# Optimization experiments

Measured on AMD Instinct MI355X. Metric: run time of the kernel, lower is better.

Reference implementation:

```python
import jax, jax.numpy as jnp
import numpy as np

HEADS, KDIM, VDIM = 8, 32, 64  # ImageLinearAttention defaults
EPS = 1e-8

def lrelu(x):
    return jax.nn.leaky_relu(x, 0.2)

def up2(x):
    # torch nn.Upsample(scale_factor=2, mode='bilinear', align_corners=False)
    b, c, h, w = x.shape
    return jax.image.resize(x, (b, c, 2 * h, 2 * w), method='bilinear')

def blur(x):
    # normalized [1,2,1] outer-product depthwise blur (kornia filter2d, normalized=True)
    c = x.shape[1]
    f = jnp.array([1.0, 2.0, 1.0], dtype=x.dtype)
    k = (f[:, None] * f[None, :]) / 16.0
    kern = jnp.broadcast_to(k, (c, 1, 3, 3))
    return jax.lax.conv_general_dilated(x, kern, (1, 1), [(1, 1), (1, 1)], feature_group_count=c)

def conv2dmod(x, W, y, demod):
    # x [b,ci,h,w], W [co,ci,k,k], y [b,ci]; per-sample modulated (de)conv
    w = W[None] * (y[:, None, :, None, None] + 1.0)  # [b,co,ci,k,k]
    if demod:
        d = jax.lax.rsqrt(jnp.sum(w * w, axis=(2, 3, 4), keepdims=True) + EPS)
        w = w * d
    pad = (W.shape[-1] - 1) // 2  # same padding, stride=1, dilation=1
    conv1 = lambda xi, wi: jax.lax.conv_general_dilated(xi[None], wi, (1, 1), [(pad, pad), (pad, pad)])[0]
    return jax.vmap(conv1)(x, w)

def attn_and_ff(x, qw, kw, vw, ow, ob, ga, f1w, f1b, f2w, f2b, gf):
    # Residual(Rezero(ImageLinearAttention)) then Residual(Rezero(conv1x1-leaky-conv1x1))
    b, c, h, w = x.shape
    n = h * w
    xf = x.reshape(b, c, n)
    scale = KDIM ** -0.25
    q = (jnp.einsum('dc,bcn->bdn', qw, xf) * scale).reshape(b, HEADS, KDIM, n)
    k = (jnp.einsum('dc,bcn->bdn', kw, xf) * scale).reshape(b, HEADS, KDIM, n)
    v = jnp.einsum('dc,bcn->bdn', vw, xf).reshape(b, HEADS, VDIM, n)
    k = jax.nn.softmax(k, axis=-1)          # over pixels
    q = jax.nn.softmax(q, axis=-2)          # norm_queries: over key dim
    ctx = jnp.einsum('bhdn,bhen->bhde', k, v)
    out = jnp.einsum('bhdn,bhde->bhen', q, ctx).reshape(b, HEADS * VDIM, n)
    out = jnp.einsum('cd,bdn->bcn', ow, out) + ob[None, :, None]
    x = x + ga * out.reshape(b, c, h, w)
    h1 = lrelu(jnp.einsum('dc,bcn->bdn', f1w, x.reshape(b, c, n)) + f1b[None, :, None])
    ff = jnp.einsum('cd,bdn->bcn', f2w, h1) + f2b[None, :, None]
    return x + gf * ff.reshape(b, c, h, w)

def setup_inputs() -> dict:
    key = jax.random.key(0)
    ks = jax.random.split(key, 20)
    B, CIN, F, L, H, W = 4, 128, 64, 512, 64, 64
    DK, DV = HEADS * KDIM, HEADS * VDIM
    d = {}
    d['x'] = jax.random.normal(ks[0], (B, CIN, H, W), jnp.float32)
    d['prev_rgb'] = jax.random.normal(ks[1], (B, 3, 2 * H, 2 * W), jnp.float32)
    d['istyle'] = jax.random.normal(ks[2], (B, L), jnp.float32)
    d['noise1'] = jax.random.normal(ks[3], (B, F, 2 * H, 2 * W), jnp.float32)
    d['noise2'] = jax.random.normal(ks[4], (B, F, 2 * H, 2 * W), jnp.float32)
    d['conv1_w'] = jax.random.normal(ks[5], (F, CIN, 3, 3), jnp.float32) * (2.0 / (CIN * 9)) ** 0.5
    d['conv2_w'] = jax.random.normal(ks[6], (F, F, 3, 3), jnp.float32) * (2.0 / (F * 9)) ** 0.5
    d['style_w'] = jax.random.normal(ks[7], (F, L), jnp.float32) * L ** -0.5
    d['style_b'] = jnp.zeros((F,), jnp.float32)
    d['rgb_w'] = jax.random.normal(ks[8], (3, F, 1, 1), jnp.float32) * (2.0 / F) ** 0.5
    d['qw'] = jax.random.normal(ks[9], (2, DK, F), jnp.float32) * F ** -0.5
    d['kw'] = jax.random.normal(ks[10], (2, DK, F), jnp.float32) * F ** -0.5
    d['vw'] = jax.random.normal(ks[11], (2, DV, F), jnp.float32) * F ** -0.5
    d['ow'] = jax.random.normal(ks[12], (2, F, DV), jnp.float32) * DV ** -0.5
    d['ob'] = jnp.zeros((2, F), jnp.float32)
    d['ga'] = 0.1 * jnp.ones((2,), jnp.float32)  # rezero gate (nonzero for a meaningful baseline)
    d['f1w'] = jax.random.normal(ks[13], (2, 2 * F, F), jnp.float32) * F ** -0.5
    d['f1b'] = jnp.zeros((2, 2 * F), jnp.float32)
    d['f2w'] = jax.random.normal(ks[14], (2, F, 2 * F), jnp.float32) * (2 * F) ** -0.5
    d['f2b'] = jnp.zeros((2, F), jnp.float32)
    d['gf'] = 0.1 * jnp.ones((2,), jnp.float32)
    return d

def reference(x, prev_rgb, istyle, noise1, noise2, conv1_w, conv2_w, style_w, style_b, rgb_w,
              qw, kw, vw, ow, ob, ga, f1w, f1b, f2w, f2b, gf):
    b = x.shape[0]
    x = up2(x)
    n1 = attn_and_ff(noise1, qw[0], kw[0], vw[0], ow[0], ob[0], ga[0], f1w[0], f1b[0], f2w[0], f2b[0], gf[0])
    n2 = attn_and_ff(noise2, qw[1], kw[1], vw[1], ow[1], ob[1], ga[1], f1w[1], f1b[1], f2w[1], f2b[1], gf[1])
    ones1 = jnp.ones((b, conv1_w.shape[1]), x.dtype)  # style1 = ones
    x = lrelu(conv2dmod(x, conv1_w, ones1, True) + n1)
    ones2 = jnp.ones((b, conv2_w.shape[1]), x.dtype)  # style2 = ones
    x = lrelu(conv2dmod(x, conv2_w, ones2, True) + n2)
    style = istyle @ style_w.T + style_b             # RGBBlock.to_style
    rgb = conv2dmod(x, rgb_w, style, False) + prev_rgb
    rgb = blur(up2(rgb))                             # upsample_rgb: bilinear x2 + blur
    return (x, rgb)
```

## Files before the change

kernel.cpp:

```cpp
#include <hip/hip_runtime.h>
#include <math.h>

#define NB 4
#define NF 64
#define NPIX 16384
#define DK 256
#define DV 512
#define QKSCALE 0.4204482f

typedef __attribute__((ext_vector_type(8))) short bf16x8;
typedef __attribute__((ext_vector_type(4))) float f32x4;
#define MFMA16(a, b, c) __builtin_amdgcn_mfma_f32_16x16x32_bf16(a, b, c, 0, 0, 0)

__device__ __forceinline__ short f2bf(float f) {
  __bf16 h = (__bf16)f;
  return __builtin_bit_cast(short, h);
}
__device__ __forceinline__ float bf2f(short s) {
  unsigned u = ((unsigned)(unsigned short)s) << 16;
  return __builtin_bit_cast(float, u);
}

#define OFF_XUPT   0L
#define OFF_XAT    4194304L
#define OFF_NBT    6291456L
#define OFF_NZT    10485760L
#define OFF_GPART  14680064L
#define OFF_WB1    25165824L
#define OFF_WB2    25202688L
#define OFF_STYLE  25221120L
#define OFF_RGBS   25221376L
#define OFF_QWB    25417984L
#define OFF_KWB    25434368L
#define OFF_F1WB   25450752L
#define OFF_F2WB   25458944L
#define OFF_MTT    25467136L
#define OFF_GSUM   25532672L

#define CDIV(a,b) (((a)+(b)-1)/(b))

__global__ void cvt4_kernel(const float* __restrict__ qw, const float* __restrict__ kw,
                            const float* __restrict__ f1w, const float* __restrict__ f2w,
                            short* __restrict__ qwP, short* __restrict__ kwP,
                            short* __restrict__ f1P, short* __restrict__ f2P,
                            const float* __restrict__ istyle, const float* __restrict__ sw,
                            const float* __restrict__ sb, float* __restrict__ styleb) {
  if (blockIdx.x == 384) {
    int b = threadIdx.x >> 6;
    int c = threadIdx.x & 63;
    float a = 0.f;
    const float* ip = istyle + b * 512;
    const float* wp = sw + c * 512;
    for (int l = 0; l < 512; ++l) a += ip[l] * wp[l];
    styleb[b * 64 + c] = a + sb[c];
    return;
  }
  int i = blockIdx.x * 256 + threadIdx.x;
  if (i < 32768) {
    int i_t = i >> 14, rem = i & 16383;
    int hd = rem >> 10, ks = (rem >> 9) & 1, lane = (rem >> 3) & 63, j = rem & 7;
    int l15 = lane & 15, quad = lane >> 4;
    qwP[i] = f2bf(qw[i_t * 16384 + (hd * 16 + l15) * 64 + ks * 32 + quad * 8 + j]);
  } else if (i < 65536) {
    int ii = i - 32768;
    int i_t = ii >> 14, rem = ii & 16383;
    int q = rem >> 12, dt = (rem >> 10) & 3, ks = (rem >> 9) & 1, lane = (rem >> 3) & 63, j = rem & 7;
    int l15 = lane & 15, quad = lane >> 4;
    kwP[ii] = f2bf(kw[i_t * 16384 + (q * 64 + dt * 16 + l15) * 64 + ks * 32 + quad * 8 + j]);
  } else if (i < 81920) {
    int ii = i - 65536;
    int i_t = ii >> 13, rem = ii & 8191;
    int jt = rem >> 10, ks = (rem >> 9) & 1, lane = (rem >> 3) & 63, j = rem & 7;
    int l15 = lane & 15, quad = lane >> 4;
    f1P[ii] = f2bf(f1w[i_t * 8192 + (jt * 16 + l15) * 64 + ks * 32 + quad * 8 + j]);
  } else {
    int ii = i - 81920;
    int i_t = ii >> 13, rem = ii & 8191;
    int ct = rem >> 11, p = (rem >> 10) & 1, ks = (rem >> 9) & 1, lane = (rem >> 3) & 63, j = rem & 7;
    int l15 = lane & 15, quad = lane >> 4;
    f2P[ii] = f2bf(f2w[i_t * 8192 + (ct * 16 + l15) * 128 + p * 64 + ks * 32 + quad * 8 + j]);
  }
}

__global__ __launch_bounds__(256) void up2t_kernel(const float* __restrict__ in,
                                                   short* __restrict__ outT) {
  __shared__ float row[64 * 132];
  int b = blockIdx.y, y = blockIdx.x, tid = threadIdx.x;
  int w = tid >> 6, lane = tid & 63, quad = lane >> 4, l15 = lane & 15;
  float iy = y * 0.5f - 0.25f;
  int y0 = (int)floorf(iy); float wy = iy - (float)y0;
  int ylo = y0 < 0 ? 0 : y0;
  int yhi = y0 + 1 > 63 ? 63 : y0 + 1;
  for (int it = 0; it < 32; ++it) {
    int idx = it * 256 + tid;
    int c = idx >> 6, xin = idx & 63;
    const float* bp = in + ((long)(b * 128 + c)) * 4096;
    float v0 = bp[ylo * 64 + xin];
    float v1 = bp[yhi * 64 + xin];
    row[xin * 132 + c] = (1.f - wy) * v0 + wy * v1;
  }
  __syncthreads();
  long ybase = (((long)(b * 128 + y)) * 128) * 128;
#pragma unroll
  for (int s = 0; s < 8; ++s) {
    int x = w * 32 + s * 4 + quad;
    float ix = x * 0.5f - 0.25f;
    int x0 = (int)floorf(ix); float wx = ix - (float)x0;
    int xlo = x0 < 0 ? 0 : x0;
    int xhi = x0 + 1 > 63 ? 63 : x0 + 1;
    bf16x8 pack;
#pragma unroll
    for (int j = 0; j < 8; ++j) {
      int c = l15 * 8 + j;
      float v = (1.f - wx) * row[xlo * 132 + c] + wx * row[xhi * 132 + c];
      pack[j] = f2bf(v);
    }
    *(bf16x8*)(outT + ybase + (long)x * 128 + l15 * 8) = pack;
  }
}

__global__ __launch_bounds__(256) void nzt_kernel(const float* __restrict__ nz1,
                                                  const float* __restrict__ nz2,
                                                  short* __restrict__ nzP) {
  __shared__ short tile[64 * 264];
  int i = blockIdx.z, b = blockIdx.y;
  long n0 = (long)blockIdx.x * 256;
  const float* nz = (i == 0) ? nz1 : nz2;
  int tid = threadIdx.x;
  const float* src = nz + (long)b * 64 * NPIX + n0;
#pragma unroll
  for (int k = 0; k < 16; ++k) {
    int idx = tid + k * 256;
    int c = idx >> 6, g = idx & 63;
    float4 v = *(const float4*)(src + (long)c * NPIX + g * 4);
    short* tp = tile + c * 264 + g * 4;
    tp[0] = f2bf(v.x); tp[1] = f2bf(v.y); tp[2] = f2bf(v.z); tp[3] = f2bf(v.w);
  }
  __syncthreads();
  long fragb = ((long)(i * NB + b)) * 1024 + blockIdx.x * 16;
#pragma unroll
  for (int v = 0; v < 8; ++v) {
    int slot = tid + v * 256;
    int frag = slot >> 6, lane = slot & 63;
    int nt = frag >> 1, ks = frag & 1;
    int l15 = lane & 15, quad = lane >> 4;
    bf16x8 pack;
#pragma unroll
    for (int j = 0; j < 8; ++j)
      pack[j] = tile[(ks * 32 + quad * 8 + j) * 264 + nt * 16 + l15];
    *(bf16x8*)(nzP + ((fragb + nt) * 2 + ks) * 512 + lane * 8) = pack;
  }
}

__global__ void wnorm2_kernel(const float* __restrict__ W1, const float* __restrict__ W2,
                              short* __restrict__ wb1, short* __restrict__ wb2) {
  int which = blockIdx.x >> 6;
  int co = blockIdx.x & 63;
  const float* W = which ? W2 : W1;
  short* wbP = which ? wb2 : wb1;
  int CI = which ? 64 : 128;
  int n = CI * 9;
  int KS = CI >> 5;
  __shared__ float red[256];
  float s = 0.f;
  for (int idx = threadIdx.x; idx < n; idx += 256) {
    float w2 = 2.0f * W[co * n + idx];
    s += w2 * w2;
  }
  red[threadIdx.x] = s;
  __syncthreads();
  for (int off = 128; off > 0; off >>= 1) {
    if (threadIdx.x < off) red[threadIdx.x] += red[threadIdx.x + off];
    __syncthreads();
  }
  float sc = rsqrtf(red[0] + 1e-8f);
  int ct = co >> 4, l15 = co & 15;
  for (int idx = threadIdx.x; idx < n; idx += 256) {
    int ci = idx / 9, k = idx - ci * 9;
    int ks = ci >> 5, quad = (ci >> 3) & 3, j = ci & 7;
    wbP[((k * 4 + ct) * KS + ks) * 512 + (quad * 16 + l15) * 8 + j] =
        f2bf(2.0f * W[co * n + idx] * sc);
  }
}

__global__ __launch_bounds__(256, 4) void pk_kernel(const float* __restrict__ nz1,
                                                    const float* __restrict__ nz2,
                                                    const short* __restrict__ nzP,
                                                    const short* __restrict__ kwP,
                                                    short* __restrict__ Gpartb) {
  __shared__ __attribute__((aligned(16))) char lds[39168];
  int bi = blockIdx.x, ch = blockIdx.y;
  int i = bi >> 2, b = bi & 3;
  const float* nz = (i == 0) ? nz1 : nz2;
  const short* kwP_i = kwP + i * (DK * NF);
  int tid = threadIdx.x;
  int w = tid >> 6, lane = tid & 63, quad = lane >> 4, l15 = lane & 15;
  int n0 = ch * 128;
  short* Xb = (short*)lds;
  short* Ph = (short*)(lds + 21760);
#pragma unroll
  for (int k = 0; k < 8; ++k) {
    int idx = tid + k * 256;
    int c = idx >> 5, g = idx & 31;
    float4 v = *(const float4*)(nz + ((long)b * 64 + c) * NPIX + n0 + g * 4);
    short* xp = Xb + c * 136 + g * 4;
    xp[0] = f2bf(v.x); xp[1] = f2bf(v.y); xp[2] = f2bf(v.z); xp[3] = f2bf(v.w);
  }
  for (int k = 0; k < 8; ++k) {
    int idx = tid + k * 256;
    int c = 64 + (idx >> 7), n = idx & 127;
    Xb[c * 136 + n] = (c == 64) ? (short)0x3F80 : (short)0;
  }
  bf16x8 bfr[2][2];
#pragma unroll
  for (int j = 0; j < 2; ++j)
#pragma unroll
    for (int ks = 0; ks < 2; ++ks)
      bfr[j][ks] = *(const bf16x8*)(nzP +
          (((long)bi * 1024 + ch * 8 + 2 * w + j) * 2 + ks) * 512 + lane * 8);
  __syncthreads();
  for (int q = 0; q < 4; ++q) {
    f32x4 acc[2][4];
#pragma unroll
    for (int j = 0; j < 2; ++j)
#pragma unroll
      for (int dt = 0; dt < 4; ++dt) acc[j][dt] = (f32x4){0.f, 0.f, 0.f, 0.f};
#pragma unroll
    for (int j = 0; j < 2; ++j) {
#pragma unroll
      for (int ks = 0; ks < 2; ++ks) {
#pragma unroll
        for (int dt = 0; dt < 4; ++dt) {
          bf16x8 afr = *(const bf16x8*)(kwP_i + (((q * 4 + dt) * 2 + ks) * 512 + lane * 8));
          acc[j][dt] = MFMA16(afr, bfr[j][ks], acc[j][dt]);
        }
      }
    }
#pragma unroll
    for (int j = 0; j < 2; ++j) {
      int ntile = 2 * w + j;
#pragma unroll
      for (int dt = 0; dt < 4; ++dt)
#pragma unroll
        for (int r = 0; r < 4; ++r) {
          float p = __expf(acc[j][dt][r] * QKSCALE);
          Ph[(dt * 16 + quad * 4 + r) * 136 + ntile * 16 + l15] = f2bf(p);
        }
    }
    __syncthreads();
#pragma unroll
    for (int ct = 0; ct < 5; ++ct) {
      f32x4 g = (f32x4){0.f, 0.f, 0.f, 0.f};
#pragma unroll
      for (int ks = 0; ks < 4; ++ks) {
        bf16x8 afr = *(const bf16x8*)(Ph + (w * 16 + l15) * 136 + ks * 32 + quad * 8);
        bf16x8 bfr2 = *(const bf16x8*)(Xb + (ct * 16 + l15) * 136 + ks * 32 + quad * 8);
        g = MFMA16(afr, bfr2, g);
      }
#pragma unroll
      for (int r = 0; r < 4; ++r) {
        int row = q * 64 + w * 16 + quad * 4 + r;
        Gpartb[(((long)bi * 128 + ch) * 256 + row) * 80 + ct * 16 + l15] = f2bf(g[r]);
      }
    }
    __syncthreads();
  }
}

__global__ __launch_bounds__(256) void gsum_kernel(const short* __restrict__ Gpartb,
                                                   float* __restrict__ Gsum) {
  int idx4 = blockIdx.x * 256 + threadIdx.x;
  int bi = idx4 / 5120;
  int rem4 = idx4 - bi * 5120;
  const short* gp = Gpartb + (long)bi * 128 * 20480 + rem4 * 4;
  float a0 = 0.f, a1 = 0.f, a2 = 0.f, a3 = 0.f;
#pragma unroll 8
  for (int ch = 0; ch < 128; ++ch) {
    short4 v = *(const short4*)(gp + (long)ch * 20480);
    a0 += bf2f(v.x); a1 += bf2f(v.y); a2 += bf2f(v.z); a3 += bf2f(v.w);
  }
  float4 o = {a0, a1, a2, a3};
  *(float4*)(Gsum + (long)bi * 20480 + rem4 * 4) = o;
}

__global__ __launch_bounds__(256) void ctxM_kernel(const float* __restrict__ Gsum,
                                                   const float* __restrict__ vw,
                                                   const float* __restrict__ ow,
                                                   short* __restrict__ MtP) {
  int i = blockIdx.z, b = blockIdx.y, dt = blockIdx.x * 16;
  int h = dt >> 5;
  __shared__ float Gs[16][81];
  __shared__ float ctxs[16][68];
  int t = threadIdx.x;
  const float* gsb = Gsum + ((long)(i * NB + b)) * 20480;
  for (int idx = t; idx < 1280; idx += 256) {
    int dl = idx / 80, c = idx - dl * 80;
    Gs[dl][c] = gsb[(dt + dl) * 80 + c];
  }
  __syncthreads();
  const float* vw_i = vw + (long)i * DV * NF;
  const float* ow_i = ow + (long)i * NF * DV;
  for (int idx = t; idx < 1024; idx += 256) {
    int dl = idx & 15, e = idx >> 4;
    const float* vp = vw_i + (h * 64 + e) * 64;
    float a = 0.f;
#pragma unroll
    for (int c = 0; c < 64; ++c) a += Gs[dl][c] * vp[c];
    ctxs[dl][e] = a / Gs[dl][64];
  }
  __syncthreads();
  short* mtp = MtP + ((long)(i * NB + b)) * 16384;
  for (int idx = t; idx < 1024; idx += 256) {
    int dl = idx & 15, c = idx >> 4;
    const float* op = ow_i + c * 512 + h * 64;
    float a = 0.f;
#pragma unroll
    for (int e = 0; e < 64; ++e) a += op[e] * ctxs[dl][e];
    int d = dt + dl;
    int ct = c >> 4, l15 = c & 15, hh = d >> 5, quad = (d >> 3) & 3, r = d & 7;
    mtp[((ct * 8 + hh) * 64 + quad * 16 + l15) * 8 + r] = f2bf(a);
  }
}

__global__ __launch_bounds__(256, 6) void attnd4_kernel(
    const short* __restrict__ nzP, const short* __restrict__ qwP,
    const short* __restrict__ MtP, const float* __restrict__ ob,
    const float* __restrict__ gap, const short* __restrict__ f1P,
    const float* __restrict__ f1b, const short* __restrict__ f2P,
    const float* __restrict__ f2b, const float* __restrict__ gfp,
    short* __restrict__ noutP) {
  __shared__ __attribute__((aligned(16))) short lds[4 * 2048];
  int bi = blockIdx.x;
  int i = bi >> 2;
  int tid = threadIdx.x;
  int w = tid >> 6, lane = tid & 63, quad = lane >> 4, l15 = lane & 15;
  short* Xt = lds + w * 2048;
  short* Es = Xt + 1152;
  float ga = gap[i], gf = gfp[i];
  const short* qwP_i = qwP + i * (DK * NF);
  const short* f1P_i = f1P + i * (128 * 64);
  const float* f1b_i = f1b + i * 128;
  const short* f2P_i = f2P + i * (64 * 128);
  const float* f2b_i = f2b + i * 64;
  const float* ob_i = ob + i * 64;
  long ntile = (long)bi * 1024 + blockIdx.y * 4 + w;
  const short* nb = nzP + ntile * 1024;
  bf16x8 xfr0 = *(const bf16x8*)(nb + lane * 8);
  bf16x8 xfr1 = *(const bf16x8*)(nb + 512 + lane * 8);
  *(bf16x8*)(Xt + l15 * 72 + quad * 8) = xfr0;
  *(bf16x8*)(Xt + l15 * 72 + 32 + quad * 8) = xfr1;
  const short* mtp = MtP + (long)bi * 16384;
  f32x4 acc2[4];
#pragma unroll
  for (int ct = 0; ct < 4; ++ct) acc2[ct] = (f32x4){0.f, 0.f, 0.f, 0.f};
#pragma unroll
  for (int h = 0; h < 8; ++h) {
    f32x4 q[2];
#pragma unroll
    for (int dd = 0; dd < 2; ++dd) {
      int hd = 2 * h + dd;
      q[dd] = (f32x4){0.f, 0.f, 0.f, 0.f};
      bf16x8 a0 = *(const bf16x8*)(qwP_i + (hd * 2 + 0) * 512 + lane * 8);
      q[dd] = MFMA16(a0, xfr0, q[dd]);
      bf16x8 a1 = *(const bf16x8*)(qwP_i + (hd * 2 + 1) * 512 + lane * 8);
      q[dd] = MFMA16(a1, xfr1, q[dd]);
    }
    float part = 0.f;
#pragma unroll
    for (int dd = 0; dd < 2; ++dd)
#pragma unroll
      for (int r = 0; r < 4; ++r) {
        float e = __expf(q[dd][r] * QKSCALE);
        q[dd][r] = e;
        part += e;
      }
    float p2 = part + __shfl_xor(part, 16);
    float s = p2 + __shfl_xor(p2, 32);
    float inv = 1.0f / s;
#pragma unroll
    for (int dd = 0; dd < 2; ++dd) {
      short4 ev;
      ev.x = f2bf(q[dd][0] * inv); ev.y = f2bf(q[dd][1] * inv);
      ev.z = f2bf(q[dd][2] * inv); ev.w = f2bf(q[dd][3] * inv);
      *(short4*)(Es + l15 * 56 + dd * 16 + quad * 4) = ev;
    }
    bf16x8 efr = *(const bf16x8*)(Es + l15 * 56 + quad * 8);
#pragma unroll
    for (int ct = 0; ct < 4; ++ct) {
      bf16x8 afr = *(const bf16x8*)(mtp + (ct * 8 + h) * 512 + lane * 8);
      acc2[ct] = MFMA16(afr, efr, acc2[ct]);
    }
  }
  float yreg[4][4];
#pragma unroll
  for (int ct = 0; ct < 4; ++ct) {
    int c0 = ct * 16 + quad * 4;
    short4 xs = *(const short4*)(Xt + l15 * 72 + c0);
    float xv[4] = {bf2f(xs.x), bf2f(xs.y), bf2f(xs.z), bf2f(xs.w)};
    short4 ys;
#pragma unroll
    for (int r = 0; r < 4; ++r) yreg[ct][r] = xv[r] + ga * (acc2[ct][r] + ob_i[c0 + r]);
    ys.x = f2bf(yreg[ct][0]); ys.y = f2bf(yreg[ct][1]);
    ys.z = f2bf(yreg[ct][2]); ys.w = f2bf(yreg[ct][3]);
    *(short4*)(Xt + l15 * 72 + c0) = ys;
  }
  bf16x8 yfr0 = *(const bf16x8*)(Xt + l15 * 72 + quad * 8);
  bf16x8 yfr1 = *(const bf16x8*)(Xt + l15 * 72 + 32 + quad * 8);
  f32x4 acc3[8];
#pragma unroll
  for (int jt = 0; jt < 8; ++jt) {
    acc3[jt] = (f32x4){0.f, 0.f, 0.f, 0.f};
    bf16x8 a0 = *(const bf16x8*)(f1P_i + (jt * 2 + 0) * 512 + lane * 8);
    acc3[jt] = MFMA16(a0, yfr0, acc3[jt]);
    bf16x8 a1 = *(const bf16x8*)(f1P_i + (jt * 2 + 1) * 512 + lane * 8);
    acc3[jt] = MFMA16(a1, yfr1, acc3[jt]);
  }
  f32x4 acc4[4];
#pragma unroll
  for (int ct = 0; ct < 4; ++ct) acc4[ct] = (f32x4){0.f, 0.f, 0.f, 0.f};
#pragma unroll
  for (int p = 0; p < 2; ++p) {
#pragma unroll
    for (int jj = 0; jj < 4; ++jj) {
      int jt = p * 4 + jj;
      short4 hs;
#pragma unroll
      for (int r = 0; r < 4; ++r) {
        float a = acc3[jt][r] + f1b_i[jt * 16 + quad * 4 + r];
        a = a > 0.f ? a : 0.2f * a;
        ((short*)&hs)[r] = f2bf(a);
      }
      *(short4*)(Xt + l15 * 72 + jj * 16 + quad * 4) = hs;
    }
    bf16x8 h0 = *(const bf16x8*)(Xt + l15 * 72 + quad * 8);
    bf16x8 h1 = *(const bf16x8*)(Xt + l15 * 72 + 32 + quad * 8);
#pragma unroll
    for (int ct = 0; ct < 4; ++ct) {
      bf16x8 a0 = *(const bf16x8*)(f2P_i + ((ct * 2 + p) * 2 + 0) * 512 + lane * 8);
      acc4[ct] = MFMA16(a0, h0, acc4[ct]);
      bf16x8 a1 = *(const bf16x8*)(f2P_i + ((ct * 2 + p) * 2 + 1) * 512 + lane * 8);
      acc4[ct] = MFMA16(a1, h1, acc4[ct]);
    }
  }
#pragma unroll
  for (int ct = 0; ct < 4; ++ct) {
    int c0 = ct * 16 + quad * 4;
    short4 ov;
#pragma unroll
    for (int r = 0; r < 4; ++r)
      ((short*)&ov)[r] = f2bf(yreg[ct][r] + gf * (acc4[ct][r] + f2b_i[c0 + r]));
    *(short4*)(noutP + (ntile * 4 + ct) * 256 + lane * 4) = ov;
  }
}

__global__ __launch_bounds__(256, 4) void convmfma_kernel(
    const short* __restrict__ inT, int CI, const short* __restrict__ wbP,
    const short* __restrict__ addnP, float* __restrict__ out_nchw,
    short* __restrict__ out_nhwc, const float* __restrict__ rgbw,
    const float* __restrict__ styleb, const float* __restrict__ prev,
    float* __restrict__ rgbs) {
  __shared__ __attribute__((aligned(16))) short Bs[3 * 66 * 40];
  int xh = blockIdx.x, y = blockIdx.y, b = blockIdx.z;
  int tid = threadIdx.x;
  int w = tid >> 6, lane = tid & 63, quad = lane >> 4, l15 = lane & 15;
  int KS = CI >> 5;
  f32x4 acc[4];
#pragma unroll
  for (int ct = 0; ct < 4; ++ct) acc[ct] = (f32x4){0.f, 0.f, 0.f, 0.f};
  for (int ks = 0; ks < KS; ++ks) {
    if (ks) __syncthreads();
    for (int t = tid; t < 792; t += 256) {
      int ci8 = t & 3, xr = t >> 2;
      int xi = xr % 66, r = xr / 66;
      int gy = y + r - 1, gx = xh * 64 + xi - 1;
      bf16x8 v = {0, 0, 0, 0, 0, 0, 0, 0};
      if (gy >= 0 && gy < 128 && gx >= 0 && gx < 128)
        v = *(const bf16x8*)(inT + (((long)(b * 128 + gy)) * 128 + gx) * CI + ks * 32 + ci8 * 8);
      *(bf16x8*)(Bs + (r * 66 + xi) * 40 + ci8 * 8) = v;
    }
    __syncthreads();
#pragma unroll
    for (int sh = 0; sh < 9; ++sh) {
      int dyv = sh / 3, dxv = sh - dyv * 3;
      const short* wbase = wbP + ((sh * 4) * KS + ks) * 512 + lane * 8;
      bf16x8 a0 = *(const bf16x8*)(wbase);
      bf16x8 a1 = *(const bf16x8*)(wbase + KS * 512);
      bf16x8 a2 = *(const bf16x8*)(wbase + 2 * KS * 512);
      bf16x8 a3 = *(const bf16x8*)(wbase + 3 * KS * 512);
      int xi = w * 16 + l15 + dxv;
      bf16x8 bf = *(const bf16x8*)(Bs + (dyv * 66 + xi) * 40 + quad * 8);
      acc[0] = MFMA16(a0, bf, acc[0]);
      acc[1] = MFMA16(a1, bf, acc[1]);
      acc[2] = MFMA16(a2, bf, acc[2]);
      acc[3] = MFMA16(a3, bf, acc[3]);
    }
  }
  int x = xh * 64 + w * 16 + l15;
  long nidx = ((long)(b * 128 + y)) * 128 + x;
  long ntile = (long)b * 1024 + y * 8 + xh * 4 + w;
  float p0 = 0.f, p1 = 0.f, p2 = 0.f;
#pragma unroll
  for (int ct = 0; ct < 4; ++ct) {
    short4 ad = *(const short4*)(addnP + (ntile * 4 + ct) * 256 + lane * 4);
    float av[4] = {bf2f(ad.x), bf2f(ad.y), bf2f(ad.z), bf2f(ad.w)};
    float v[4];
#pragma unroll
    for (int r = 0; r < 4; ++r) {
      float a = acc[ct][r] + av[r];
      v[r] = a > 0.f ? a : 0.2f * a;
    }
    if (out_nchw) {
#pragma unroll
      for (int r = 0; r < 4; ++r) {
        int co = ct * 16 + quad * 4 + r;
        out_nchw[((long)(b * 64 + co)) * 16384 + y * 128 + x] = v[r];
      }
    }
    if (out_nhwc) {
      short4 pv;
      pv.x = f2bf(v[0]); pv.y = f2bf(v[1]); pv.z = f2bf(v[2]); pv.w = f2bf(v[3]);
      *(short4*)(out_nhwc + nidx * 64 + ct * 16 + quad * 4) = pv;
    }
    if (rgbw) {
#pragma unroll
      for (int r = 0; r < 4; ++r) {
        int co = ct * 16 + quad * 4 + r;
        float mv = (styleb[b * 64 + co] + 1.0f) * v[r];
        p0 += rgbw[co] * mv;
        p1 += rgbw[64 + co] * mv;
        p2 += rgbw[128 + co] * mv;
      }
    }
  }
  if (rgbw) {
    p0 += __shfl_xor(p0, 16); p0 += __shfl_xor(p0, 32);
    p1 += __shfl_xor(p1, 16); p1 += __shfl_xor(p1, 32);
    p2 += __shfl_xor(p2, 16); p2 += __shfl_xor(p2, 32);
    if (quad == 0) {
      long pi = y * 128 + x;
      rgbs[((long)(b * 3 + 0)) * 16384 + pi] = p0 + prev[((long)(b * 3 + 0)) * 16384 + pi];
      rgbs[((long)(b * 3 + 1)) * 16384 + pi] = p1 + prev[((long)(b * 3 + 1)) * 16384 + pi];
      rgbs[((long)(b * 3 + 2)) * 16384 + pi] = p2 + prev[((long)(b * 3 + 2)) * 16384 + pi];
    }
  }
}

__global__ void upblur_kernel(const float* __restrict__ rgbs, float* __restrict__ out) {
  __shared__ float rows[3][128];
  int bc = blockIdx.y, Y = blockIdx.x, X = threadIdx.x;
  int m = Y >> 1;
  const float* base = rgbs + (long)bc * 16384;
  for (int t = X; t < 384; t += 256) {
    int sr = t >> 7, xx = t & 127;
    int rr = m - 1 + sr;
    rr = rr < 0 ? 0 : (rr > 127 ? 127 : rr);
    rows[sr][xx] = base[rr * 128 + xx];
  }
  __syncthreads();
  const float w3[3] = {1.f, 2.f, 1.f};
  float s = 0.f;
#pragma unroll
  for (int dy = -1; dy <= 1; ++dy) {
    int Yv = Y + dy;
    if (Yv < 0 || Yv > 255) continue;
    float iy = Yv * 0.5f - 0.25f;
    int y0 = (int)floorf(iy); float wy = iy - (float)y0;
    int ylo = y0 < 0 ? 0 : y0;
    int yhi = y0 + 1 > 127 ? 127 : y0 + 1;
    int slo = ylo - m + 1, shi = yhi - m + 1;
#pragma unroll
    for (int dx = -1; dx <= 1; ++dx) {
      int Xv = X + dx;
      if (Xv < 0 || Xv > 255) continue;
      float ix = Xv * 0.5f - 0.25f;
      int x0 = (int)floorf(ix); float wx = ix - (float)x0;
      int xlo = x0 < 0 ? 0 : x0;
      int xhi = x0 + 1 > 127 ? 127 : x0 + 1;
      float v = (1.f - wy) * ((1.f - wx) * rows[slo][xlo] + wx * rows[slo][xhi])
              + wy * ((1.f - wx) * rows[shi][xlo] + wx * rows[shi][xhi]);
      s += w3[dy + 1] * w3[dx + 1] * v;
    }
  }
  out[(long)bc * 65536 + Y * 256 + X] = s * (1.0f / 16.0f);
}

extern "C" void kernel_launch(void* const* d_in, const int* in_sizes, int n_in,
                              void* d_out, int out_size, void* d_ws, size_t ws_size,
                              hipStream_t stream) {
  (void)in_sizes; (void)n_in; (void)out_size; (void)ws_size;
  const float* x        = (const float*)d_in[0];
  const float* prev_rgb = (const float*)d_in[1];
  const float* istyle   = (const float*)d_in[2];
  const float* noise1   = (const float*)d_in[3];
  const float* noise2   = (const float*)d_in[4];
  const float* conv1_w  = (const float*)d_in[5];
  const float* conv2_w  = (const float*)d_in[6];
  const float* style_w  = (const float*)d_in[7];
  const float* style_b  = (const float*)d_in[8];
  const float* rgb_w    = (const float*)d_in[9];
  const float* qw       = (const float*)d_in[10];
  const float* kw       = (const float*)d_in[11];
  const float* vw       = (const float*)d_in[12];
  const float* ow       = (const float*)d_in[13];
  const float* ob       = (const float*)d_in[14];
  const float* ga       = (const float*)d_in[15];
  const float* f1w      = (const float*)d_in[16];
  const float* f1b      = (const float*)d_in[17];
  const float* f2w      = (const float*)d_in[18];
  const float* f2b      = (const float*)d_in[19];
  const float* gf       = (const float*)d_in[20];
  float* out_x   = (float*)d_out;
  float* out_rgb = out_x + 4194304;
  float* ws = (float*)d_ws;

  short* xupT   = (short*)(ws + OFF_XUPT);
  short* xaT    = (short*)(ws + OFF_XAT);
  short* nbufP  = (short*)(ws + OFF_NBT);
  short* nzP    = (short*)(ws + OFF_NZT);
  short* Gpartb = (short*)(ws + OFF_GPART);
  short* wb1    = (short*)(ws + OFF_WB1);
  short* wb2    = (short*)(ws + OFF_WB2);
  float* styleb = ws + OFF_STYLE;
  float* rgbs   = ws + OFF_RGBS;
  short* qwP    = (short*)(ws + OFF_QWB);
  short* kwP    = (short*)(ws + OFF_KWB);
  short* f1P    = (short*)(ws + OFF_F1WB);
  short* f2P    = (short*)(ws + OFF_F2WB);
  short* MtP    = (short*)(ws + OFF_MTT);
  float* Gsum   = ws + OFF_GSUM;

  cvt4_kernel<<<385, 256, 0, stream>>>(qw, kw, f1w, f2w, qwP, kwP, f1P, f2P,
                                       istyle, style_w, style_b, styleb);
  wnorm2_kernel<<<128, 256, 0, stream>>>(conv1_w, conv2_w, wb1, wb2);
  up2t_kernel<<<dim3(128, NB), 256, 0, stream>>>(x, xupT);
  nzt_kernel<<<dim3(64, NB, 2), 256, 0, stream>>>(noise1, noise2, nzP);

  pk_kernel<<<dim3(8, 128), 256, 0, stream>>>(noise1, noise2, nzP, kwP, Gpartb);
  gsum_kernel<<<160, 256, 0, stream>>>(Gpartb, Gsum);
  ctxM_kernel<<<dim3(16, NB, 2), 256, 0, stream>>>(Gsum, vw, ow, MtP);
  attnd4_kernel<<<dim3(8, 256), 256, 0, stream>>>(nzP, qwP, MtP, ob, ga,
                                                  f1P, f1b, f2P, f2b, gf, nbufP);

  convmfma_kernel<<<dim3(2, 128, NB), 256, 0, stream>>>(
      xupT, 128, wb1, nbufP, nullptr, xaT, nullptr, nullptr, nullptr, nullptr);
  convmfma_kernel<<<dim3(2, 128, NB), 256, 0, stream>>>(
      xaT, 64, wb2, nbufP + 4194304L, out_x, nullptr, rgb_w, styleb, prev_rgb, rgbs);

  upblur_kernel<<<dim3(256, 12), 256, 0, stream>>>(rgbs, out_rgb);
}
```

Baseline: 298.1 us.

## Merge prep kernels into one launch and build noise fragments inside pk_kernel

Combines the weight conversion, style, weight demodulation and upsample-transpose kernels into a single prep_kernel, dispatched by block index. The separate noise transpose kernel is removed: pk_kernel now writes the bf16 MFMA fragments of noise to nzP from its own LDS tile and reads its B fragments from LDS rather than global memory. This saves three launches and one full read pass over the noise tensors. In exchange, pk_kernel gains an extra barrier and strided LDS gathers, and the fused prep kernel reserves its largest LDS footprint for every block.

```diff
diff --git a/kernel.cpp b/kernel.cpp
--- a/kernel.cpp
+++ b/kernel.cpp
@@ -39,15 +39,50 @@
 
 #define CDIV(a,b) (((a)+(b)-1)/(b))
 
-__global__ void cvt4_kernel(const float* __restrict__ qw, const float* __restrict__ kw,
-                            const float* __restrict__ f1w, const float* __restrict__ f2w,
-                            short* __restrict__ qwP, short* __restrict__ kwP,
-                            short* __restrict__ f1P, short* __restrict__ f2P,
-                            const float* __restrict__ istyle, const float* __restrict__ sw,
-                            const float* __restrict__ sb, float* __restrict__ styleb) {
-  if (blockIdx.x == 384) {
-    int b = threadIdx.x >> 6;
-    int c = threadIdx.x & 63;
+__global__ __launch_bounds__(256) void prep_kernel(
+    const float* __restrict__ qw, const float* __restrict__ kw,
+    const float* __restrict__ f1w, const float* __restrict__ f2w,
+    short* __restrict__ qwP, short* __restrict__ kwP,
+    short* __restrict__ f1P, short* __restrict__ f2P,
+    const float* __restrict__ istyle, const float* __restrict__ sw,
+    const float* __restrict__ sb, float* __restrict__ styleb,
+    const float* __restrict__ W1, const float* __restrict__ W2,
+    short* __restrict__ wb1, short* __restrict__ wb2,
+    const float* __restrict__ xin, short* __restrict__ xupT) {
+  __shared__ float shmem[64 * 132];
+  int bid = blockIdx.x;
+  int tid = threadIdx.x;
+  if (bid < 384) {
+    int i = bid * 256 + tid;
+    if (i < 32768) {
+      int i_t = i >> 14, rem = i & 16383;
+      int hd = rem >> 10, ks = (rem >> 9) & 1, lane = (rem >> 3) & 63, j = rem & 7;
+      int l15 = lane & 15, quad = lane >> 4;
+      qwP[i] = f2bf(qw[i_t * 16384 + (hd * 16 + l15) * 64 + ks * 32 + quad * 8 + j]);
+    } else if (i < 65536) {
+      int ii = i - 32768;
+      int i_t = ii >> 14, rem = ii & 16383;
+      int q = rem >> 12, dt = (rem >> 10) & 3, ks = (rem >> 9) & 1, lane = (rem >> 3) & 63, j = rem & 7;
+      int l15 = lane & 15, quad = lane >> 4;
+      kwP[ii] = f2bf(kw[i_t * 16384 + (q * 64 + dt * 16 + l15) * 64 + ks * 32 + quad * 8 + j]);
+    } else if (i < 81920) {
+      int ii = i - 65536;
+      int i_t = ii >> 13, rem = ii & 8191;
+      int jt = rem >> 10, ks = (rem >> 9) & 1, lane = (rem >> 3) & 63, j = rem & 7;
+      int l15 = lane & 15, quad = lane >> 4;
+      f1P[ii] = f2bf(f1w[i_t * 8192 + (jt * 16 + l15) * 64 + ks * 32 + quad * 8 + j]);
+    } else {
+      int ii = i - 81920;
+      int i_t = ii >> 13, rem = ii & 8191;
+      int ct = rem >> 11, p = (rem >> 10) & 1, ks = (rem >> 9) & 1, lane = (rem >> 3) & 63, j = rem & 7;
+      int l15 = lane & 15, quad = lane >> 4;
+      f2P[ii] = f2bf(f2w[i_t * 8192 + (ct * 16 + l15) * 128 + p * 64 + ks * 32 + quad * 8 + j]);
+    }
+    return;
+  }
+  if (bid == 384) {
+    int b = tid >> 6;
+    int c = tid & 63;
     float a = 0.f;
     const float* ip = istyle + b * 512;
     const float* wp = sw + c * 512;
@@ -55,49 +90,52 @@
     styleb[b * 64 + c] = a + sb[c];
     return;
   }
-  int i = blockIdx.x * 256 + threadIdx.x;
-  if (i < 32768) {
-    int i_t = i >> 14, rem = i & 16383;
-    int hd = rem >> 10, ks = (rem >> 9) & 1, lane = (rem >> 3) & 63, j = rem & 7;
-    int l15 = lane & 15, quad = lane >> 4;
-    qwP[i] = f2bf(qw[i_t * 16384 + (hd * 16 + l15) * 64 + ks * 32 + quad * 8 + j]);
-  } else if (i < 65536) {
-    int ii = i - 32768;
-    int i_t = ii >> 14, rem = ii & 16383;
-    int q = rem >> 12, dt = (rem >> 10) & 3, ks = (rem >> 9) & 1, lane = (rem >> 3) & 63, j = rem & 7;
-    int l15 = lane & 15, quad = lane >> 4;
-    kwP[ii] = f2bf(kw[i_t * 16384 + (q * 64 + dt * 16 + l15) * 64 + ks * 32 + quad * 8 + j]);
-  } else if (i < 81920) {
-    int ii = i - 65536;
-    int i_t = ii >> 13, rem = ii & 8191;
-    int jt = rem >> 10, ks = (rem >> 9) & 1, lane = (rem >> 3) & 63, j = rem & 7;
-    int l15 = lane & 15, quad = lane >> 4;
-    f1P[ii] = f2bf(f1w[i_t * 8192 + (jt * 16 + l15) * 64 + ks * 32 + quad * 8 + j]);
-  } else {
-    int ii = i - 81920;
-    int i_t = ii >> 13, rem = ii & 8191;
-    int ct = rem >> 11, p = (rem >> 10) & 1, ks = (rem >> 9) & 1, lane = (rem >> 3) & 63, j = rem & 7;
-    int l15 = lane & 15, quad = lane >> 4;
-    f2P[ii] = f2bf(f2w[i_t * 8192 + (ct * 16 + l15) * 128 + p * 64 + ks * 32 + quad * 8 + j]);
-  }
-}
-
-__global__ __launch_bounds__(256) void up2t_kernel(const float* __restrict__ in,
-                                                   short* __restrict__ outT) {
-  __shared__ float row[64 * 132];
-  int b = blockIdx.y, y = blockIdx.x, tid = threadIdx.x;
+  if (bid < 513) {
+    int wb_ = bid - 385;
+    int which = wb_ >> 6;
+    int co = wb_ & 63;
+    const float* W = which ? W2 : W1;
+    short* wbP = which ? wb2 : wb1;
+    int CI = which ? 64 : 128;
+    int n = CI * 9;
+    int KS = CI >> 5;
+    float* red = shmem;
+    float s = 0.f;
+    for (int idx = tid; idx < n; idx += 256) {
+      float w2 = 2.0f * W[co * n + idx];
+      s += w2 * w2;
+    }
+    red[tid] = s;
+    __syncthreads();
+    for (int off = 128; off > 0; off >>= 1) {
+      if (tid < off) red[tid] += red[tid + off];
+      __syncthreads();
+    }
+    float sc = rsqrtf(red[0] + 1e-8f);
+    int ct = co >> 4, l15 = co & 15;
+    for (int idx = tid; idx < n; idx += 256) {
+      int ci = idx / 9, k = idx - ci * 9;
+      int ks = ci >> 5, quad = (ci >> 3) & 3, j = ci & 7;
+      wbP[((k * 4 + ct) * KS + ks) * 512 + (quad * 16 + l15) * 8 + j] =
+          f2bf(2.0f * W[co * n + idx] * sc);
+    }
+    return;
+  }
+  int idx0 = bid - 513;
+  int b = idx0 >> 7, y = idx0 & 127;
   int w = tid >> 6, lane = tid & 63, quad = lane >> 4, l15 = lane & 15;
+  float* row = shmem;
   float iy = y * 0.5f - 0.25f;
   int y0 = (int)floorf(iy); float wy = iy - (float)y0;
   int ylo = y0 < 0 ? 0 : y0;
   int yhi = y0 + 1 > 63 ? 63 : y0 + 1;
   for (int it = 0; it < 32; ++it) {
     int idx = it * 256 + tid;
-    int c = idx >> 6, xin = idx & 63;
-    const float* bp = in + ((long)(b * 128 + c)) * 4096;
-    float v0 = bp[ylo * 64 + xin];
-    float v1 = bp[yhi * 64 + xin];
-    row[xin * 132 + c] = (1.f - wy) * v0 + wy * v1;
+    int c = idx >> 6, xi = idx & 63;
+    const float* bp = xin + ((long)(b * 128 + c)) * 4096;
+    float v0 = bp[ylo * 64 + xi];
+    float v1 = bp[yhi * 64 + xi];
+    row[xi * 132 + c] = (1.f - wy) * v0 + wy * v1;
   }
   __syncthreads();
   long ybase = (((long)(b * 128 + y)) * 128) * 128;
@@ -115,77 +153,13 @@
       float v = (1.f - wx) * row[xlo * 132 + c] + wx * row[xhi * 132 + c];
       pack[j] = f2bf(v);
     }
-    *(bf16x8*)(outT + ybase + (long)x * 128 + l15 * 8) = pack;
-  }
-}
-
-__global__ __launch_bounds__(256) void nzt_kernel(const float* __restrict__ nz1,
-                                                  const float* __restrict__ nz2,
-                                                  short* __restrict__ nzP) {
-  __shared__ short tile[64 * 264];
-  int i = blockIdx.z, b = blockIdx.y;
-  long n0 = (long)blockIdx.x * 256;
-  const float* nz = (i == 0) ? nz1 : nz2;
-  int tid = threadIdx.x;
-  const float* src = nz + (long)b * 64 * NPIX + n0;
-#pragma unroll
-  for (int k = 0; k < 16; ++k) {
-    int idx = tid + k * 256;
-    int c = idx >> 6, g = idx & 63;
-    float4 v = *(const float4*)(src + (long)c * NPIX + g * 4);
-    short* tp = tile + c * 264 + g * 4;
-    tp[0] = f2bf(v.x); tp[1] = f2bf(v.y); tp[2] = f2bf(v.z); tp[3] = f2bf(v.w);
-  }
-  __syncthreads();
-  long fragb = ((long)(i * NB + b)) * 1024 + blockIdx.x * 16;
-#pragma unroll
-  for (int v = 0; v < 8; ++v) {
-    int slot = tid + v * 256;
-    int frag = slot >> 6, lane = slot & 63;
-    int nt = frag >> 1, ks = frag & 1;
-    int l15 = lane & 15, quad = lane >> 4;
-    bf16x8 pack;
-#pragma unroll
-    for (int j = 0; j < 8; ++j)
-      pack[j] = tile[(ks * 32 + quad * 8 + j) * 264 + nt * 16 + l15];
-    *(bf16x8*)(nzP + ((fragb + nt) * 2 + ks) * 512 + lane * 8) = pack;
-  }
-}
-
-__global__ void wnorm2_kernel(const float* __restrict__ W1, const float* __restrict__ W2,
-                              short* __restrict__ wb1, short* __restrict__ wb2) {
-  int which = blockIdx.x >> 6;
-  int co = blockIdx.x & 63;
-  const float* W = which ? W2 : W1;
-  short* wbP = which ? wb2 : wb1;
-  int CI = which ? 64 : 128;
-  int n = CI * 9;
-  int KS = CI >> 5;
-  __shared__ float red[256];
-  float s = 0.f;
-  for (int idx = threadIdx.x; idx < n; idx += 256) {
-    float w2 = 2.0f * W[co * n + idx];
-    s += w2 * w2;
-  }
-  red[threadIdx.x] = s;
-  __syncthreads();
-  for (int off = 128; off > 0; off >>= 1) {
-    if (threadIdx.x < off) red[threadIdx.x] += red[threadIdx.x + off];
-    __syncthreads();
-  }
-  float sc = rsqrtf(red[0] + 1e-8f);
-  int ct = co >> 4, l15 = co & 15;
-  for (int idx = threadIdx.x; idx < n; idx += 256) {
-    int ci = idx / 9, k = idx - ci * 9;
-    int ks = ci >> 5, quad = (ci >> 3) & 3, j = ci & 7;
-    wbP[((k * 4 + ct) * KS + ks) * 512 + (quad * 16 + l15) * 8 + j] =
-        f2bf(2.0f * W[co * n + idx] * sc);
+    *(bf16x8*)(xupT + ybase + (long)x * 128 + l15 * 8) = pack;
   }
 }
 
 __global__ __launch_bounds__(256, 4) void pk_kernel(const float* __restrict__ nz1,
                                                     const float* __restrict__ nz2,
-                                                    const short* __restrict__ nzP,
+                                                    short* __restrict__ nzP,
                                                     const short* __restrict__ kwP,
                                                     short* __restrict__ Gpartb) {
   __shared__ __attribute__((aligned(16))) char lds[39168];
@@ -211,14 +185,28 @@
     int c = 64 + (idx >> 7), n = idx & 127;
     Xb[c * 136 + n] = (c == 64) ? (short)0x3F80 : (short)0;
   }
+  __syncthreads();
+  long fragb = (long)bi * 1024 + ch * 8;
+#pragma unroll
+  for (int v = 0; v < 4; ++v) {
+    int slot = tid + v * 256;
+    int frag = slot >> 6, ln = slot & 63;
+    int nt = frag >> 1, ksf = frag & 1;
+    int fl15 = ln & 15, fq = ln >> 4;
+    bf16x8 pack;
+#pragma unroll
+    for (int j = 0; j < 8; ++j)
+      pack[j] = Xb[(ksf * 32 + fq * 8 + j) * 136 + nt * 16 + fl15];
+    *(bf16x8*)(nzP + ((fragb + nt) * 2 + ksf) * 512 + ln * 8) = pack;
+  }
   bf16x8 bfr[2][2];
 #pragma unroll
   for (int j = 0; j < 2; ++j)
 #pragma unroll
     for (int ks = 0; ks < 2; ++ks)
-      bfr[j][ks] = *(const bf16x8*)(nzP +
-          (((long)bi * 1024 + ch * 8 + 2 * w + j) * 2 + ks) * 512 + lane * 8);
-  __syncthreads();
+#pragma unroll
+      for (int jj = 0; jj < 8; ++jj)
+        bfr[j][ks][jj] = Xb[(ks * 32 + quad * 8 + jj) * 136 + (2 * w + j) * 16 + l15];
   for (int q = 0; q < 4; ++q) {
     f32x4 acc[2][4];
 #pragma unroll
@@ -629,11 +617,9 @@
   short* MtP    = (short*)(ws + OFF_MTT);
   float* Gsum   = ws + OFF_GSUM;
 
-  cvt4_kernel<<<385, 256, 0, stream>>>(qw, kw, f1w, f2w, qwP, kwP, f1P, f2P,
-                                       istyle, style_w, style_b, styleb);
-  wnorm2_kernel<<<128, 256, 0, stream>>>(conv1_w, conv2_w, wb1, wb2);
-  up2t_kernel<<<dim3(128, NB), 256, 0, stream>>>(x, xupT);
-  nzt_kernel<<<dim3(64, NB, 2), 256, 0, stream>>>(noise1, noise2, nzP);
+  prep_kernel<<<1025, 256, 0, stream>>>(qw, kw, f1w, f2w, qwP, kwP, f1P, f2P,
+                                        istyle, style_w, style_b, styleb,
+                                        conv1_w, conv2_w, wb1, wb2, x, xupT);
 
   pk_kernel<<<dim3(8, 128), 256, 0, stream>>>(noise1, noise2, nzP, kwP, Gpartb);
   gsum_kernel<<<160, 256, 0, stream>>>(Gpartb, Gsum);
```

Result: faster. 280.0 us (-6.1%).
